# Kernel optimization log

Hardware: AMD Instinct MI355X
Metric: run time of the kernel (lower is better)

Reference implementation:

```python
import jax, jax.numpy as jnp
import numpy as np

N, E, A, D, B = 30000, 60000, 6, 16, 4096
F_IN, F_HID, F_EMB = 256, 256, 256
ALPHA = 0.2  # LeakyReLU negative slope


def _layer(node_embs, edge_embs, edge_list, node_list, Wn, We, ae, an, concat):
    out = Wn.shape[1]
    hn = node_embs @ Wn                      # [N, out]
    he = edge_embs @ We                      # [E, out]
    # stage 1: hyperedge update = attention over its member nodes
    gn = hn[edge_list]                       # [E, A, out] gather
    se = (he @ ae[:out])[:, None] + gn @ ae[out:]            # [E, A]
    att_e = jax.nn.softmax(jax.nn.leaky_relu(se, ALPHA), axis=1)
    new_edge = jnp.einsum('ea,eao->eo', att_e, gn)           # [E, out]
    # stage 2: node update = attention over its incident hyperedges
    ge = new_edge[node_list]                 # [N, D, out] gather
    sn = (hn @ an[:out])[:, None] + ge @ an[out:]            # [N, D]
    att_n = jax.nn.softmax(jax.nn.leaky_relu(sn, ALPHA), axis=1)
    new_node = jnp.einsum('nd,ndo->no', att_n, ge)           # [N, out]
    if concat:
        return jax.nn.elu(new_node), jax.nn.elu(new_edge)
    return new_node, new_edge


def setup_inputs() -> dict:
    key = jax.random.key(0)
    ks = jax.random.split(key, 16)
    s = 0.1
    return {
        'batch_inputs': jax.random.randint(ks[0], (B, A + 1), 0, N),
        'node_embs': jax.random.normal(ks[1], (N, F_IN), jnp.float32),
        'edge_embs': jax.random.normal(ks[2], (E, F_IN), jnp.float32),
        'edge_list': jax.random.randint(ks[3], (E, A), 0, N),
        'node_list': jax.random.randint(ks[4], (N, D), 0, E),
        'Wn1': jax.random.normal(ks[5], (F_IN, F_HID), jnp.float32) * s,
        'We1': jax.random.normal(ks[6], (F_IN, F_HID), jnp.float32) * s,
        'ae1': jax.random.normal(ks[7], (2 * F_HID,), jnp.float32) * s,
        'an1': jax.random.normal(ks[8], (2 * F_HID,), jnp.float32) * s,
        'Wn2': jax.random.normal(ks[9], (F_HID, F_EMB), jnp.float32) * s,
        'We2': jax.random.normal(ks[10], (F_HID, F_EMB), jnp.float32) * s,
        'ae2': jax.random.normal(ks[11], (2 * F_EMB,), jnp.float32) * s,
        'an2': jax.random.normal(ks[12], (2 * F_EMB,), jnp.float32) * s,
    }


def reference(batch_inputs, node_embs, edge_embs, edge_list, node_list,
              Wn1, We1, ae1, an1, Wn2, We2, ae2, an2):
    # single attention head (nheads=1), concat=True -> ELU; dropout identity (eval)
    n1, e1 = _layer(node_embs, edge_embs, edge_list, node_list, Wn1, We1, ae1, an1, True)
    n2, e2 = _layer(n1, e1, edge_list, node_list, Wn2, We2, ae2, an2, False)
    n2, e2 = jax.nn.elu(n2), jax.nn.elu(e2)
    # assemble: slot 0 = hyperedge embedding, slots 1..right-1 = node embeddings
    S = batch_inputs.shape[1]
    cols = jnp.arange(S - 1)
    nz = batch_inputs[:, :-1] != 0
    right = jnp.max(jnp.where(nz, cols, -1), axis=1) + 1      # [B]
    pos = jnp.arange(S)
    mask = (pos[None, :] >= 1) & (pos[None, :] < right[:, None])  # [B, S]
    gathered = n2[batch_inputs]                               # [B, S, F_EMB]
    out = jnp.where(mask[:, :, None], gathered, jnp.float32(0))
    out = out.at[:, 0, :].set(e2[batch_inputs[:, 0]])
    return out
```

## Files before the change

### kernel.cpp

```cpp
#include <hip/hip_runtime.h>
#include <stdint.h>

typedef unsigned short u16;
typedef unsigned int   u32;
typedef __attribute__((ext_vector_type(8))) short bf16x8;
typedef __attribute__((ext_vector_type(4))) float f32x4;

#define N_NODES 30000
#define N_EDGES 60000
#define A_DEG   6
#define D_DEG   16
#define BATCH   4096
#define FEAT    256
#define APAD    8

__device__ __forceinline__ float bfbits2f(u32 hi){ union{u32 u; float f;} v; v.u = hi; return v.f; }
__device__ __forceinline__ float bf2f(u16 h){ return bfbits2f(((u32)h)<<16); }
__device__ __forceinline__ u16 f2bf(float f){
  union{float f; u32 u;} v; v.f = f;
  u32 u = v.u;
  return (u16)((u + 0x7fffu + ((u>>16)&1u)) >> 16);
}

struct F4 { float x,y,z,w; };
struct F8 { float v[8]; };

__device__ __forceinline__ F4 load4(const float* p){
  float4 t = *reinterpret_cast<const float4*>(p);
  F4 f; f.x=t.x; f.y=t.y; f.z=t.z; f.w=t.w; return f;
}
__device__ __forceinline__ F4 load4(const u16* p){
  uint2 u = *reinterpret_cast<const uint2*>(p);
  F4 f;
  f.x = bfbits2f(u.x<<16);
  f.y = bfbits2f(u.x & 0xffff0000u);
  f.z = bfbits2f(u.y<<16);
  f.w = bfbits2f(u.y & 0xffff0000u);
  return f;
}
__device__ __forceinline__ F8 load8(const float* p){
  float4 a = *reinterpret_cast<const float4*>(p);
  float4 b = *reinterpret_cast<const float4*>(p+4);
  F8 f; f.v[0]=a.x; f.v[1]=a.y; f.v[2]=a.z; f.v[3]=a.w;
        f.v[4]=b.x; f.v[5]=b.y; f.v[6]=b.z; f.v[7]=b.w; return f;
}
__device__ __forceinline__ F8 load8(const u16* p){
  uint4 u = *reinterpret_cast<const uint4*>(p);
  F8 f;
  f.v[0]=bfbits2f(u.x<<16); f.v[1]=bfbits2f(u.x&0xffff0000u);
  f.v[2]=bfbits2f(u.y<<16); f.v[3]=bfbits2f(u.y&0xffff0000u);
  f.v[4]=bfbits2f(u.z<<16); f.v[5]=bfbits2f(u.z&0xffff0000u);
  f.v[6]=bfbits2f(u.w<<16); f.v[7]=bfbits2f(u.w&0xffff0000u);
  return f;
}
__device__ __forceinline__ void acc8(float* o, uint4 u, float ww){
  o[0] += ww*bfbits2f(u.x<<16); o[1] += ww*bfbits2f(u.x&0xffff0000u);
  o[2] += ww*bfbits2f(u.y<<16); o[3] += ww*bfbits2f(u.y&0xffff0000u);
  o[4] += ww*bfbits2f(u.z<<16); o[5] += ww*bfbits2f(u.z&0xffff0000u);
  o[6] += ww*bfbits2f(u.w<<16); o[7] += ww*bfbits2f(u.w&0xffff0000u);
}
__device__ __forceinline__ void store_bf8(u16* p, const float* f){
  uint4 u;
  u.x = (u32)f2bf(f[0]) | ((u32)f2bf(f[1])<<16);
  u.y = (u32)f2bf(f[2]) | ((u32)f2bf(f[3])<<16);
  u.z = (u32)f2bf(f[4]) | ((u32)f2bf(f[5])<<16);
  u.w = (u32)f2bf(f[6]) | ((u32)f2bf(f[7])<<16);
  *reinterpret_cast<uint4*>(p) = u;
}

__device__ __forceinline__ float eluf(float x){ return x > 0.f ? x : (__expf(x) - 1.f); }
__device__ __forceinline__ float lrelu(float x){ return x > 0.f ? x : 0.2f*x; }

__device__ __forceinline__ float wave_sum_lane0(float v){
  #pragma unroll
  for (int off = 32; off > 0; off >>= 1) v += __shfl_down(v, off, 64);
  return v;
}
__device__ __forceinline__ float half_sum_all(float v){
  #pragma unroll
  for (int off = 1; off < 32; off <<= 1) v += __shfl_xor(v, off, 64);
  return v;
}

__global__ __launch_bounds__(256) void wtrans_k(const float* __restrict__ W1,
    u16* __restrict__ Wt1, const float* __restrict__ W2, u16* __restrict__ Wt2)
{
  const float* W = blockIdx.z ? W2 : W1;
  u16* Wt        = blockIdx.z ? Wt2 : Wt1;
  __shared__ float T[32][33];
  const int bx = blockIdx.x;
  const int by = blockIdx.y;
  const int tc = threadIdx.x & 31;
  const int tr = threadIdx.x >> 5;
  #pragma unroll
  for (int i=0;i<4;i++){
    int r = tr + i*8;
    T[r][tc] = W[(bx*32 + r)*FEAT + by*32 + tc];
  }
  __syncthreads();
  #pragma unroll
  for (int i=0;i<4;i++){
    int r = tr + i*8;
    Wt[(by*32 + r)*FEAT + bx*32 + tc] = f2bf(T[tc][r]);
  }
}

__global__ __launch_bounds__(256) void wvec_k(
    const float* __restrict__ W1, const float* __restrict__ a1, float* __restrict__ o1,
    const float* __restrict__ W2, const float* __restrict__ a2, float* __restrict__ o2)
{
  const int sel  = blockIdx.x >> 6;
  const float* W = sel ? W2 : W1;
  const float* a = sel ? a2 : a1;
  float* o       = sel ? o2 : o1;
  const int lane = threadIdx.x & 63;
  const int row  = (blockIdx.x & 63)*4 + (threadIdx.x >> 6);
  const int c = lane*4;
  F4 h = load4(W + (long)row*FEAT + c);
  F4 v = load4(a + c);
  float p = wave_sum_lane0(h.x*v.x + h.y*v.y + h.z*v.z + h.w*v.w);
  if (lane == 0) o[row] = p;
}

template<bool ELU, typename TIN>
__global__ __launch_bounds__(256) void gemm_mfma_k(
    const TIN* __restrict__ X, const u16* __restrict__ Wt,
    const float* __restrict__ v1, const float* __restrict__ v2,
    u16* __restrict__ Y, float* __restrict__ hg, float* __restrict__ snb,
    int M)
{
  __shared__ u16 As[64][FEAT + APAD];
  __shared__ float hgs[64], sns[64];
  const int tid = threadIdx.x;
  const long row0 = (long)blockIdx.x * 64;

  if (tid < 64){ hgs[tid] = 0.f; sns[tid] = 0.f; }

  {
    const int c = (tid & 15) << 4;
    #pragma unroll
    for (int i=0;i<4;i++){
      const int r = (tid >> 4) + 16*i;
      u16* dst = &As[r][c];
      if (row0 + r < M){
        const TIN* src = X + (row0 + r)*FEAT + c;
        #pragma unroll
        for (int j=0;j<4;j++){
          F4 v = load4(src + 4*j);
          if (ELU){ v.x=eluf(v.x); v.y=eluf(v.y); v.z=eluf(v.z); v.w=eluf(v.w); }
          dst[4*j+0]=f2bf(v.x); dst[4*j+1]=f2bf(v.y);
          dst[4*j+2]=f2bf(v.z); dst[4*j+3]=f2bf(v.w);
        }
      } else {
        #pragma unroll
        for (int j=0;j<16;j++) dst[j] = 0;
      }
    }
  }
  __syncthreads();

  const int wave = tid >> 6;
  const int lane = tid & 63;
  const int l15  = lane & 15;
  const int kg   = lane >> 4;

  f32x4 acc[4][4] = {};

  for (int k0 = 0; k0 < FEAT; k0 += 32){
    bf16x8 a[4], b[4];
    #pragma unroll
    for (int rt=0;rt<4;rt++)
      a[rt] = *reinterpret_cast<const bf16x8*>(&As[rt*16 + l15][k0 + kg*8]);
    #pragma unroll
    for (int t=0;t<4;t++){
      const int n = wave*64 + t*16 + l15;
      b[t] = *reinterpret_cast<const bf16x8*>(Wt + (long)n*FEAT + k0 + kg*8);
    }
    #pragma unroll
    for (int rt=0;rt<4;rt++)
      #pragma unroll
      for (int t=0;t<4;t++)
        acc[rt][t] = __builtin_amdgcn_mfma_f32_16x16x32_bf16(a[rt], b[t], acc[rt][t], 0, 0, 0);
  }

  __syncthreads();

  float p1[4][4] = {}, p2[4][4] = {};
  #pragma unroll
  for (int t=0;t<4;t++){
    const int col = wave*64 + t*16 + l15;
    const float a1 = v1[col];
    const float a2 = v2[col];
    #pragma unroll
    for (int rt=0;rt<4;rt++){
      #pragma unroll
      for (int r=0;r<4;r++){
        const float val = acc[rt][t][r];
        As[rt*16 + kg*4 + r][col] = f2bf(val);
        p1[rt][r] += val * a1;
        p2[rt][r] += val * a2;
      }
    }
  }
  #pragma unroll
  for (int off=1; off<16; off<<=1){
    #pragma unroll
    for (int rt=0;rt<4;rt++)
      #pragma unroll
      for (int r=0;r<4;r++){
        p1[rt][r] += __shfl_xor(p1[rt][r], off, 64);
        p2[rt][r] += __shfl_xor(p2[rt][r], off, 64);
      }
  }
  if (l15 == 0){
    #pragma unroll
    for (int rt=0;rt<4;rt++)
      #pragma unroll
      for (int r=0;r<4;r++){
        atomicAdd(&hgs[rt*16 + kg*4 + r], p1[rt][r]);
        atomicAdd(&sns[rt*16 + kg*4 + r], p2[rt][r]);
      }
  }
  __syncthreads();

  {
    const int c = (tid & 15) << 4;
    #pragma unroll
    for (int i=0;i<4;i++){
      const int r = (tid >> 4) + 16*i;
      if (row0 + r < M){
        const uint4* s = reinterpret_cast<const uint4*>(&As[r][c]);
        uint4* d = reinterpret_cast<uint4*>(Y + (row0 + r)*FEAT + c);
        d[0] = s[0]; d[1] = s[1];
      }
    }
  }
  if (tid < 64 && row0 + tid < M){
    hg[row0 + tid]  = hgs[tid];
    snb[row0 + tid] = sns[tid];
  }
}

__global__ __launch_bounds__(256) void node_gemm_k(
    const u16* __restrict__ NE, const int* __restrict__ node_list,
    const float* __restrict__ snb1, const float* __restrict__ ned,
    const u16* __restrict__ Wt,
    const float* __restrict__ v1, const float* __restrict__ v2,
    u16* __restrict__ Y, float* __restrict__ hg, float* __restrict__ snb2,
    int M)
{
  __shared__ u16 As[64][FEAT + APAD];
  __shared__ float hgs[64], sns[64];
  const int tid = threadIdx.x;
  const long row0 = (long)blockIdx.x * 64;

  if (tid < 64){ hgs[tid] = 0.f; sns[tid] = 0.f; }

  const int hw = tid >> 5;
  const int hl = tid & 31;
  const int c  = hl*8;
  #pragma unroll
  for (int i=0;i<8;i++){
    const int r = hw*8 + i;
    const long n = row0 + r;
    u16* dst = &As[r][c];
    if (n < M){
      int idx[D_DEG];
      #pragma unroll
      for (int d=0; d<D_DEG; d++) idx[d] = node_list[n*D_DEG + d];
      float nv[D_DEG];
      #pragma unroll
      for (int d=0; d<D_DEG; d++) nv[d] = ned[idx[d]];
      const float sb = snb1[n];
      float w[D_DEG];
      float mx = -1e30f;
      #pragma unroll
      for (int d=0; d<D_DEG; d++){
        float s = lrelu(sb + nv[d]);
        w[d] = s; mx = fmaxf(mx, s);
      }
      float sum = 0.f;
      #pragma unroll
      for (int d=0; d<D_DEG; d++){ w[d] = __expf(w[d]-mx); sum += w[d]; }
      const float inv = 1.f/sum;

      uint4 hb[D_DEG];
      #pragma unroll
      for (int d=0; d<D_DEG; d++)
        hb[d] = *reinterpret_cast<const uint4*>(NE + (long)idx[d]*FEAT + c);
      float o[8] = {};
      #pragma unroll
      for (int d=0; d<D_DEG; d++) acc8(o, hb[d], w[d]*inv);

      #pragma unroll
      for (int j=0;j<8;j++) dst[j] = f2bf(eluf(o[j]));
    } else {
      #pragma unroll
      for (int j=0;j<8;j++) dst[j] = 0;
    }
  }
  __syncthreads();

  const int wave = tid >> 6;
  const int lane = tid & 63;
  const int l15  = lane & 15;
  const int kg   = lane >> 4;

  f32x4 acc[4][4] = {};

  for (int k0 = 0; k0 < FEAT; k0 += 32){
    bf16x8 a[4], b[4];
    #pragma unroll
    for (int rt=0;rt<4;rt++)
      a[rt] = *reinterpret_cast<const bf16x8*>(&As[rt*16 + l15][k0 + kg*8]);
    #pragma unroll
    for (int t=0;t<4;t++){
      const int n = wave*64 + t*16 + l15;
      b[t] = *reinterpret_cast<const bf16x8*>(Wt + (long)n*FEAT + k0 + kg*8);
    }
    #pragma unroll
    for (int rt=0;rt<4;rt++)
      #pragma unroll
      for (int t=0;t<4;t++)
        acc[rt][t] = __builtin_amdgcn_mfma_f32_16x16x32_bf16(a[rt], b[t], acc[rt][t], 0, 0, 0);
  }

  __syncthreads();

  float p1[4][4] = {}, p2[4][4] = {};
  #pragma unroll
  for (int t=0;t<4;t++){
    const int col = wave*64 + t*16 + l15;
    const float a1 = v1[col];
    const float a2 = v2[col];
    #pragma unroll
    for (int rt=0;rt<4;rt++){
      #pragma unroll
      for (int r=0;r<4;r++){
        const float val = acc[rt][t][r];
        As[rt*16 + kg*4 + r][col] = f2bf(val);
        p1[rt][r] += val * a1;
        p2[rt][r] += val * a2;
      }
    }
  }
  #pragma unroll
  for (int off=1; off<16; off<<=1){
    #pragma unroll
    for (int rt=0;rt<4;rt++)
      #pragma unroll
      for (int r=0;r<4;r++){
        p1[rt][r] += __shfl_xor(p1[rt][r], off, 64);
        p2[rt][r] += __shfl_xor(p2[rt][r], off, 64);
      }
  }
  if (l15 == 0){
    #pragma unroll
    for (int rt=0;rt<4;rt++)
      #pragma unroll
      for (int r=0;r<4;r++){
        atomicAdd(&hgs[rt*16 + kg*4 + r], p1[rt][r]);
        atomicAdd(&sns[rt*16 + kg*4 + r], p2[rt][r]);
      }
  }
  __syncthreads();

  {
    const int cc = (tid & 15) << 4;
    #pragma unroll
    for (int i=0;i<4;i++){
      const int r = (tid >> 4) + 16*i;
      if (row0 + r < M){
        const uint4* s = reinterpret_cast<const uint4*>(&As[r][cc]);
        uint4* d = reinterpret_cast<uint4*>(Y + (row0 + r)*FEAT + cc);
        d[0] = s[0]; d[1] = s[1];
      }
    }
  }
  if (tid < 64 && row0 + tid < M){
    hg[row0 + tid]   = hgs[tid];
    snb2[row0 + tid] = sns[tid];
  }
}

template<typename TIN, bool ELU>
__global__ __launch_bounds__(256) void edge_attn_k(const u16* __restrict__ Hn,
    const TIN* __restrict__ Xe, const float* __restrict__ wE,
    const int* __restrict__ edge_list,
    const float* __restrict__ hg, const float* __restrict__ an_hi,
    u16* __restrict__ NE, float* __restrict__ ned)
{
  const int tid = threadIdx.x;
  const int hl  = tid & 31;
  const int e   = blockIdx.x*8 + (tid >> 5);
  const int c   = hl*8;

  int idx[A_DEG];
  #pragma unroll
  for (int a=0;a<A_DEG;a++) idx[a] = edge_list[e*A_DEG + a];
  float hgv[A_DEG];
  #pragma unroll
  for (int a=0;a<A_DEG;a++) hgv[a] = hg[idx[a]];
  uint4 hb[A_DEG];
  #pragma unroll
  for (int a=0;a<A_DEG;a++)
    hb[a] = *reinterpret_cast<const uint4*>(Hn + (long)idx[a]*FEAT + c);

  float sb;
  {
    F8 x = load8(Xe + (long)e*FEAT + c);
    if (ELU){
      #pragma unroll
      for (int j=0;j<8;j++) x.v[j] = eluf(x.v[j]);
    }
    F8 v = load8(wE + c);
    float p = 0.f;
    #pragma unroll
    for (int j=0;j<8;j++) p += x.v[j]*v.v[j];
    sb = half_sum_all(p);
  }

  float w[A_DEG];
  float mx = -1e30f;
  #pragma unroll
  for (int a=0;a<A_DEG;a++){
    float s = lrelu(sb + hgv[a]);
    w[a] = s; mx = fmaxf(mx, s);
  }
  float sum = 0.f;
  #pragma unroll
  for (int a=0;a<A_DEG;a++){ w[a] = __expf(w[a]-mx); sum += w[a]; }
  const float inv = 1.f/sum;

  float o[8] = {};
  #pragma unroll
  for (int a=0;a<A_DEG;a++) acc8(o, hb[a], w[a]*inv);
  store_bf8(NE + (long)e*FEAT + c, o);

  F8 v = load8(an_hi + c);
  float p = 0.f;
  #pragma unroll
  for (int j=0;j<8;j++) p += o[j]*v.v[j];
  p = half_sum_all(p);
  if (hl == 0) ned[e] = p;
}

__global__ __launch_bounds__(256) void node_attn_k(const u16* __restrict__ NE,
    const int* __restrict__ node_list, const float* __restrict__ snb,
    const float* __restrict__ ned, u16* __restrict__ NNo)
{
  const int tid = threadIdx.x;
  const int hl  = tid & 31;
  const int n   = blockIdx.x*8 + (tid >> 5);
  const int c   = hl*8;

  int idx[D_DEG];
  #pragma unroll
  for (int d=0; d<D_DEG; d++) idx[d] = node_list[n*D_DEG + d];
  float nv[D_DEG];
  #pragma unroll
  for (int d=0; d<D_DEG; d++) nv[d] = ned[idx[d]];

  const float sb = snb[n];
  float w[D_DEG];
  float mx = -1e30f;
  #pragma unroll
  for (int d=0; d<D_DEG; d++){
    float s = lrelu(sb + nv[d]);
    w[d] = s; mx = fmaxf(mx, s);
  }
  float sum = 0.f;
  #pragma unroll
  for (int d=0; d<D_DEG; d++){ w[d] = __expf(w[d]-mx); sum += w[d]; }
  const float inv = 1.f/sum;

  uint4 hb[D_DEG];
  #pragma unroll
  for (int d=0; d<D_DEG; d++)
    hb[d] = *reinterpret_cast<const uint4*>(NE + (long)idx[d]*FEAT + c);
  float o[8] = {};
  #pragma unroll
  for (int d=0; d<D_DEG; d++) acc8(o, hb[d], w[d]*inv);
  store_bf8(NNo + (long)n*FEAT + c, o);
}

__global__ __launch_bounds__(256) void assemble_k(const u16* __restrict__ NNo,
    const u16* __restrict__ NE, const int* __restrict__ batch, float* __restrict__ out)
{
  const int b = blockIdx.x;
  const int j = threadIdx.x;
  int bi[7];
  #pragma unroll
  for (int s=0;s<7;s++) bi[s] = batch[b*7 + s];
  int right = 0;
  #pragma unroll
  for (int c=0;c<6;c++) if (bi[c] != 0) right = c+1;

  out[((long)b*7 + 0)*FEAT + j] = eluf(bf2f(NE[(long)bi[0]*FEAT + j]));

  #pragma unroll
  for (int s=1;s<7;s++){
    float val = 0.f;
    if (s < right) val = eluf(bf2f(NNo[(long)bi[s]*FEAT + j]));
    out[((long)b*7 + s)*FEAT + j] = val;
  }
}

extern "C" void kernel_launch(void* const* d_in, const int* in_sizes, int n_in,
                              void* d_out, int out_size, void* d_ws, size_t ws_size,
                              hipStream_t stream)
{
  const int*   batch      = (const int*)d_in[0];
  const float* node_embs  = (const float*)d_in[1];
  const float* edge_embs  = (const float*)d_in[2];
  const int*   edge_list  = (const int*)d_in[3];
  const int*   node_list  = (const int*)d_in[4];
  const float* Wn1 = (const float*)d_in[5];
  const float* We1 = (const float*)d_in[6];
  const float* ae1 = (const float*)d_in[7];
  const float* an1 = (const float*)d_in[8];
  const float* Wn2 = (const float*)d_in[9];
  const float* We2 = (const float*)d_in[10];
  const float* ae2 = (const float*)d_in[11];
  const float* an2 = (const float*)d_in[12];
  float* out = (float*)d_out;

  char* ws = (char*)d_ws;
  size_t off = 0;
  auto alloc = [&](size_t bytes)->void* {
    void* p = ws + off; off += (bytes + 255) & ~(size_t)255; return p;
  };
  u16* bHn = (u16*)alloc((size_t)N_NODES*FEAT*2);
  u16* bNE = (u16*)alloc((size_t)N_EDGES*FEAT*2);
  u16* bNN = (u16*)alloc((size_t)N_NODES*FEAT*2);
  u16* Wt1 = (u16*)alloc((size_t)FEAT*FEAT*2);
  u16* Wt2 = (u16*)alloc((size_t)FEAT*FEAT*2);
  float* hg  = (float*)alloc((size_t)N_NODES*4);
  float* snb = (float*)alloc((size_t)N_NODES*4);
  float* ned = (float*)alloc((size_t)N_EDGES*4);
  float* wE1 = (float*)alloc(FEAT*4);
  float* wE2 = (float*)alloc(FEAT*4);

  dim3 blk(256);
  const int gemm_grid = (N_NODES + 63) / 64;

  wtrans_k<<<dim3(8,8,2), blk, 0, stream>>>(Wn1, Wt1, Wn2, Wt2);
  wvec_k<<<128, blk, 0, stream>>>(We1, ae1, wE1, We2, ae2, wE2);

  gemm_mfma_k<false,float><<<gemm_grid, blk, 0, stream>>>(node_embs, Wt1,
      ae1+FEAT, an1, bHn, hg, snb, N_NODES);
  edge_attn_k<float,false><<<N_EDGES/8, blk, 0, stream>>>(bHn, edge_embs, wE1,
      edge_list, hg, an1+FEAT, bNE, ned);

  node_gemm_k<<<gemm_grid, blk, 0, stream>>>(bNE, node_list, snb, ned,
      Wt2, ae2+FEAT, an2, bHn, hg, snb, N_NODES);

  edge_attn_k<u16,true><<<N_EDGES/8, blk, 0, stream>>>(bHn, bNE, wE2,
      edge_list, hg, an2+FEAT, bNE, ned);
  node_attn_k<<<N_NODES/8, blk, 0, stream>>>(bNE, node_list, snb, ned, bNN);

  assemble_k<<<BATCH, blk, 0, stream>>>(bNN, bNE, batch, out);
}
```

Before: 303.6 us.

## Fuse final node attention into assemble and compute only batch-referenced nodes

Replaces the full-graph layer-2 node attention kernel and the separate assemble kernel with one kernel that computes node attention only for nodes referenced by batch slots that are kept. This removes the intermediate node-embedding buffer write and read, plus one launch. Duplicate node references in the batch are now recomputed, and blocks with masked slots leave some warps idle.

After: 288.0 us. 5.2% less time.

```diff
diff --git a/kernel.cpp b/kernel.cpp
--- a/kernel.cpp
+++ b/kernel.cpp
@@ -445,64 +445,72 @@
   if (hl == 0) ned[e] = p;
 }
 
-__global__ __launch_bounds__(256) void node_attn_k(const u16* __restrict__ NE,
-    const int* __restrict__ node_list, const float* __restrict__ snb,
-    const float* __restrict__ ned, u16* __restrict__ NNo)
-{
+__global__ __launch_bounds__(256) void node_assemble_k(
+    const u16* __restrict__ NE, const int* __restrict__ node_list,
+    const float* __restrict__ snb, const float* __restrict__ ned,
+    const int* __restrict__ batch, float* __restrict__ out)
+{
+  const int b   = blockIdx.x;
   const int tid = threadIdx.x;
+  const int hw  = tid >> 5;
   const int hl  = tid & 31;
-  const int n   = blockIdx.x*8 + (tid >> 5);
   const int c   = hl*8;
 
-  int idx[D_DEG];
-  #pragma unroll
-  for (int d=0; d<D_DEG; d++) idx[d] = node_list[n*D_DEG + d];
-  float nv[D_DEG];
-  #pragma unroll
-  for (int d=0; d<D_DEG; d++) nv[d] = ned[idx[d]];
-
-  const float sb = snb[n];
-  float w[D_DEG];
-  float mx = -1e30f;
-  #pragma unroll
-  for (int d=0; d<D_DEG; d++){
-    float s = lrelu(sb + nv[d]);
-    w[d] = s; mx = fmaxf(mx, s);
-  }
-  float sum = 0.f;
-  #pragma unroll
-  for (int d=0; d<D_DEG; d++){ w[d] = __expf(w[d]-mx); sum += w[d]; }
-  const float inv = 1.f/sum;
-
-  uint4 hb[D_DEG];
-  #pragma unroll
-  for (int d=0; d<D_DEG; d++)
-    hb[d] = *reinterpret_cast<const uint4*>(NE + (long)idx[d]*FEAT + c);
-  float o[8] = {};
-  #pragma unroll
-  for (int d=0; d<D_DEG; d++) acc8(o, hb[d], w[d]*inv);
-  store_bf8(NNo + (long)n*FEAT + c, o);
-}
-
-__global__ __launch_bounds__(256) void assemble_k(const u16* __restrict__ NNo,
-    const u16* __restrict__ NE, const int* __restrict__ batch, float* __restrict__ out)
-{
-  const int b = blockIdx.x;
-  const int j = threadIdx.x;
-  int bi[7];
-  #pragma unroll
-  for (int s=0;s<7;s++) bi[s] = batch[b*7 + s];
   int right = 0;
   #pragma unroll
-  for (int c=0;c<6;c++) if (bi[c] != 0) right = c+1;
-
-  out[((long)b*7 + 0)*FEAT + j] = eluf(bf2f(NE[(long)bi[0]*FEAT + j]));
-
-  #pragma unroll
-  for (int s=1;s<7;s++){
-    float val = 0.f;
-    if (s < right) val = eluf(bf2f(NNo[(long)bi[s]*FEAT + j]));
-    out[((long)b*7 + s)*FEAT + j] = val;
+  for (int cc=0; cc<6; cc++){ if (batch[b*7 + cc] != 0) right = cc+1; }
+
+  if (hw == 6){
+    const int e = batch[b*7 + 0];
+    F8 x = load8(NE + (long)e*FEAT + c);
+    float4 o0, o1;
+    o0.x=eluf(x.v[0]); o0.y=eluf(x.v[1]); o0.z=eluf(x.v[2]); o0.w=eluf(x.v[3]);
+    o1.x=eluf(x.v[4]); o1.y=eluf(x.v[5]); o1.z=eluf(x.v[6]); o1.w=eluf(x.v[7]);
+    float* po = out + ((long)b*7 + 0)*FEAT + c;
+    *reinterpret_cast<float4*>(po)   = o0;
+    *reinterpret_cast<float4*>(po+4) = o1;
+  } else if (hw < 6){
+    const int s  = hw + 1;
+    float* po = out + ((long)b*7 + s)*FEAT + c;
+    if (s < right){
+      const int n = batch[b*7 + s];
+      int idx[D_DEG];
+      #pragma unroll
+      for (int d=0; d<D_DEG; d++) idx[d] = node_list[(long)n*D_DEG + d];
+      float nv[D_DEG];
+      #pragma unroll
+      for (int d=0; d<D_DEG; d++) nv[d] = ned[idx[d]];
+      const float sb = snb[n];
+      float w[D_DEG];
+      float mx = -1e30f;
+      #pragma unroll
+      for (int d=0; d<D_DEG; d++){
+        float sc = lrelu(sb + nv[d]);
+        w[d] = sc; mx = fmaxf(mx, sc);
+      }
+      float sum = 0.f;
+      #pragma unroll
+      for (int d=0; d<D_DEG; d++){ w[d] = __expf(w[d]-mx); sum += w[d]; }
+      const float inv = 1.f/sum;
+
+      uint4 hb[D_DEG];
+      #pragma unroll
+      for (int d=0; d<D_DEG; d++)
+        hb[d] = *reinterpret_cast<const uint4*>(NE + (long)idx[d]*FEAT + c);
+      float o[8] = {};
+      #pragma unroll
+      for (int d=0; d<D_DEG; d++) acc8(o, hb[d], w[d]*inv);
+
+      float4 o0, o1;
+      o0.x=eluf(o[0]); o0.y=eluf(o[1]); o0.z=eluf(o[2]); o0.w=eluf(o[3]);
+      o1.x=eluf(o[4]); o1.y=eluf(o[5]); o1.z=eluf(o[6]); o1.w=eluf(o[7]);
+      *reinterpret_cast<float4*>(po)   = o0;
+      *reinterpret_cast<float4*>(po+4) = o1;
+    } else {
+      float4 z; z.x=0.f; z.y=0.f; z.z=0.f; z.w=0.f;
+      *reinterpret_cast<float4*>(po)   = z;
+      *reinterpret_cast<float4*>(po+4) = z;
+    }
   }
 }
 
@@ -532,7 +540,6 @@
   };
   u16* bHn = (u16*)alloc((size_t)N_NODES*FEAT*2);
   u16* bNE = (u16*)alloc((size_t)N_EDGES*FEAT*2);
-  u16* bNN = (u16*)alloc((size_t)N_NODES*FEAT*2);
   u16* Wt1 = (u16*)alloc((size_t)FEAT*FEAT*2);
   u16* Wt2 = (u16*)alloc((size_t)FEAT*FEAT*2);
   float* hg  = (float*)alloc((size_t)N_NODES*4);
@@ -557,7 +564,6 @@
 
   edge_attn_k<u16,true><<<N_EDGES/8, blk, 0, stream>>>(bHn, bNE, wE2,
       edge_list, hg, an2+FEAT, bNE, ned);
-  node_attn_k<<<N_NODES/8, blk, 0, stream>>>(bNE, node_list, snb, ned, bNN);
-
-  assemble_k<<<BATCH, blk, 0, stream>>>(bNN, bNE, batch, out);
-}
+
+  node_assemble_k<<<BATCH, blk, 0, stream>>>(bNE, node_list, snb, ned, batch, out);
+}
```
